# Kernel tuning notes

Measured on AMD Instinct MI355X. Metric: run time of the kernel, lower is better.

Reference implementation:

```python
import jax, jax.numpy as jnp
import numpy as np

STRIDE = 1
PADDING = 1
DILATION = 1


def setup_inputs() -> dict:
    key = jax.random.key(0)
    k1, k2 = jax.random.split(key)
    N, C_in, H, W = 32, 128, 56, 56
    C_out, ksz = 256, 3
    x = jax.random.normal(k1, (N, C_in, H, W), dtype=jnp.float32)
    # xavier_normal_ with gain sqrt(2): std = gain*sqrt(2/(fan_in+fan_out))
    fan_in = C_in * ksz * ksz
    fan_out = C_out * ksz * ksz
    std = np.sqrt(2.0) * np.sqrt(2.0 / (fan_in + fan_out))
    weight = jax.random.normal(k2, (C_out, C_in, ksz, ksz), dtype=jnp.float32) * jnp.float32(std)
    bias = jnp.zeros((C_out,), dtype=jnp.float32)
    return {"x": x, "weight": weight, "bias": bias}


def reference(x, weight, bias):
    # Faithful to conv2d(X, K, stride, padding, dilation, bias):
    # unfold (im2col) + matmul + fold is mathematically a standard cross-correlation
    # conv; expressed here with the efficient lax primitive.
    y = jax.lax.conv_general_dilated(
        x, weight,
        window_strides=(STRIDE, STRIDE),
        padding=[(PADDING, PADDING), (PADDING, PADDING)],
        rhs_dilation=(DILATION, DILATION),
        dimension_numbers=("NCHW", "OIHW", "NCHW"),
    )
    return y + bias[None, :, None, None]
```

## Files before the change

kernel.cpp:

```cpp
#include <hip/hip_runtime.h>
#include <hip/hip_bf16.h>


#define CIN   128
#define HH    56
#define WW    56
#define COUT  256
#define HW    3136
#define NIMG  32
#define NP    (NIMG * HW)
#define XPW   58
#define XPIX  (XPW * XPW)
#define XPAD_BYTES (NIMG * XPIX * CIN * 2)
#define WT_OFF     XPAD_BYTES

typedef __bf16 bf16x8 __attribute__((ext_vector_type(8)));
typedef float  f32x4  __attribute__((ext_vector_type(4)));

#define GLD16(g, l) __builtin_amdgcn_global_load_lds( \
    (const __attribute__((address_space(1))) void*)(g), \
    (__attribute__((address_space(3))) void*)(l), 16, 0, 0)

__device__ __forceinline__ unsigned pack_bf16(float a, float b) {
    return (__float_as_uint(b) & 0xFFFF0000u) | (__float_as_uint(a) >> 16);
}

__global__ __launch_bounds__(128) void prep_x(const float* __restrict__ x,
                                              __hip_bfloat16* __restrict__ xp) {
    __shared__ unsigned short t[HH * CIN];
    const int b  = blockIdx.x;
    const int n  = b / HH;
    const int y  = b - n * HH;
    const int ci = threadIdx.x;

    const float* src = x + ((size_t)(n * CIN + ci) * HW) + y * WW;
    #pragma unroll
    for (int j = 0; j < 14; ++j) {
        const float4 v = ((const float4*)src)[j];
        t[(4 * j + 0) * CIN + ci] = (unsigned short)(__float_as_uint(v.x) >> 16);
        t[(4 * j + 1) * CIN + ci] = (unsigned short)(__float_as_uint(v.y) >> 16);
        t[(4 * j + 2) * CIN + ci] = (unsigned short)(__float_as_uint(v.z) >> 16);
        t[(4 * j + 3) * CIN + ci] = (unsigned short)(__float_as_uint(v.w) >> 16);
    }

    const uint4 z = make_uint4(0, 0, 0, 0);
    if (ci < 32) {
        const int side = ci >> 4;
        const int j    = ci & 15;
        ((uint4*)(xp + ((size_t)n * XPIX + (y + 1) * XPW + side * 57) * CIN))[j] = z;
    }
    if (y == 0)
        for (int j = ci; j < 928; j += 128)
            ((uint4*)(xp + (size_t)n * XPIX * CIN))[j] = z;
    if (y == HH - 1)
        for (int j = ci; j < 928; j += 128)
            ((uint4*)(xp + ((size_t)n * XPIX + 57 * XPW) * CIN))[j] = z;

    __syncthreads();

    uint4* dst = (uint4*)(xp + ((size_t)n * XPIX + (y + 1) * XPW + 1) * CIN);
    const uint4* lsrc = (const uint4*)t;
    #pragma unroll
    for (int j = 0; j < 7; ++j)
        dst[j * 128 + ci] = lsrc[j * 128 + ci];
}

__global__ __launch_bounds__(256) void prep_w(const float* __restrict__ w,
                                              __hip_bfloat16* __restrict__ wt) {
    const int co = blockIdx.x * 2 + (threadIdx.x >> 7);
    const int ci = threadIdx.x & 127;
    const float* src = w + (size_t)(co * CIN + ci) * 9;
    #pragma unroll
    for (int tp = 0; tp < 9; ++tp)
        wt[(size_t)tp * (COUT * CIN) + co * CIN + ci] = __float2bfloat16(src[tp]);
}

__global__ __launch_bounds__(256) void conv_main(
    const char* __restrict__ xpb,
    const char* __restrict__ wtb,
    const float* __restrict__ bias,
    float* __restrict__ out)
{
    __shared__ __align__(16) char Alds[32768];
    __shared__ __align__(16) char Blds[32768];

    const int tid  = threadIdx.x;
    const int l    = tid & 63;
    const int wv   = tid >> 6;
    const int wm   = wv & 1;
    const int wn   = wv >> 1;
    const int l15  = l & 15;
    const int quad = l >> 4;

    const int idx = blockIdx.x;
    const int bm  = (idx >> 3) & 1;
    const int bn  = (idx >> 4) * 8 + (idx & 7);
    const int pbase  = bn * 128;
    const int cobase = bm * 128;

    unsigned aoff[8], boff[8];
    #pragma unroll
    for (int j = 0; j < 8; ++j) {
        const int c    = wv * 8 + j;
        const int row  = 4 * c + (l >> 4);
        const int gseg = (l & 15) ^ (row & 15);
        aoff[j] = (unsigned)((cobase + row) * 256 + gseg * 16);
        const int p   = pbase + row;
        const int n   = p / HW;
        const int rem = p - n * HW;
        const int y   = rem / WW;
        const int x   = rem - y * WW;
        boff[j] = (unsigned)((n * XPIX + y * XPW + x) * 256 + gseg * 16);
    }

    f32x4 acc[4][4];
    #pragma unroll
    for (int i = 0; i < 4; ++i)
        #pragma unroll
        for (int j = 0; j < 4; ++j)
            acc[i][j] = (f32x4){0.f, 0.f, 0.f, 0.f};

    #pragma unroll
    for (int t = 0; t < 9; ++t) {
        const int r = t / 3;
        const int s = t - 3 * r;
        const unsigned wo = (unsigned)(t * (COUT * CIN * 2));
        const unsigned bo = (unsigned)((r * XPW + s) * 256);

        __syncthreads();
        #pragma unroll
        for (int j = 0; j < 8; ++j) {
            const int c = wv * 8 + j;
            GLD16(wtb + wo + aoff[j], Alds + c * 1024);
            GLD16(xpb + bo + boff[j], Blds + c * 1024);
        }
        __syncthreads();

        #pragma unroll
        for (int kg = 0; kg < 4; ++kg) {
            bf16x8 af[4], bfr[4];
            #pragma unroll
            for (int mt = 0; mt < 4; ++mt) {
                const int row  = wm * 64 + mt * 16 + l15;
                const int segl = (kg * 4 + quad) ^ l15;
                af[mt] = *(const bf16x8*)(Alds + row * 256 + segl * 16);
            }
            #pragma unroll
            for (int nt = 0; nt < 4; ++nt) {
                const int row  = wn * 64 + nt * 16 + l15;
                const int segl = (kg * 4 + quad) ^ l15;
                bfr[nt] = *(const bf16x8*)(Blds + row * 256 + segl * 16);
            }
            #pragma unroll
            for (int mt = 0; mt < 4; ++mt)
                #pragma unroll
                for (int nt = 0; nt < 4; ++nt)
                    acc[mt][nt] = __builtin_amdgcn_mfma_f32_16x16x32_bf16(
                        af[mt], bfr[nt], acc[mt][nt], 0, 0, 0);
        }
    }

    #pragma unroll
    for (int nt = 0; nt < 4; ++nt) {
        const int pp = pbase + wn * 64 + nt * 16 + l15;
        const int n2 = pp / HW;
        const int r2 = pp - n2 * HW;
        float* ob = out + (size_t)n2 * (COUT * HW) + r2;
        #pragma unroll
        for (int mt = 0; mt < 4; ++mt) {
            const int co = cobase + wm * 64 + mt * 16 + quad * 4;
            const float4 bv = *(const float4*)(bias + co);
            f32x4 a = acc[mt][nt];
            ob[(size_t)(co + 0) * HW] = a[0] + bv.x;
            ob[(size_t)(co + 1) * HW] = a[1] + bv.y;
            ob[(size_t)(co + 2) * HW] = a[2] + bv.z;
            ob[(size_t)(co + 3) * HW] = a[3] + bv.w;
        }
    }
}

extern "C" void kernel_launch(void* const* d_in, const int* in_sizes, int n_in,
                              void* d_out, int out_size, void* d_ws, size_t ws_size,
                              hipStream_t stream) {
    const float* x = (const float*)d_in[0];
    const float* w = (const float*)d_in[1];
    const float* b = (const float*)d_in[2];
    char* ws = (char*)d_ws;
    __hip_bfloat16* xp = (__hip_bfloat16*)ws;
    __hip_bfloat16* wt = (__hip_bfloat16*)(ws + WT_OFF);

    prep_x<<<dim3(NIMG * HH), dim3(128), 0, stream>>>(x, xp);
    prep_w<<<dim3(128), dim3(256), 0, stream>>>(w, wt);
    conv_main<<<dim3((NP / 128) * 2), dim3(256), 0, stream>>>(
        (const char*)xp, (const char*)wt, b, (float*)d_out);
}
```

Measured before the change: 209.9 us.

## Pipeline conv K-loop with 4-stage LDS ring buffer and async loads

```diff
diff --git a/kernel.cpp b/kernel.cpp
--- a/kernel.cpp
+++ b/kernel.cpp
@@ -81,8 +81,7 @@
     const float* __restrict__ bias,
     float* __restrict__ out)
 {
-    __shared__ __align__(16) char Alds[32768];
-    __shared__ __align__(16) char Blds[32768];
+    __shared__ __align__(16) char L[65536];
 
     const int tid  = threadIdx.x;
     const int l    = tid & 63;
@@ -98,12 +97,12 @@
     const int pbase  = bn * 128;
     const int cobase = bm * 128;
 
-    unsigned aoff[8], boff[8];
-    #pragma unroll
-    for (int j = 0; j < 8; ++j) {
-        const int c    = wv * 8 + j;
-        const int row  = 4 * c + (l >> 4);
-        const int gseg = (l & 15) ^ (row & 15);
+    const int gseg = (l & 3) ^ ((l >> 3) & 3);
+    unsigned aoff[2], boff[2];
+    #pragma unroll
+    for (int j = 0; j < 2; ++j) {
+        const int c   = wv * 2 + j;
+        const int row = c * 16 + (l >> 2);
         aoff[j] = (unsigned)((cobase + row) * 256 + gseg * 16);
         const int p   = pbase + row;
         const int n   = p / HW;
@@ -112,6 +111,7 @@
         const int x   = rem - y * WW;
         boff[j] = (unsigned)((n * XPIX + y * XPW + x) * 256 + gseg * 16);
     }
+    const int segoff = (quad ^ ((l15 >> 1) & 3)) << 4;
 
     f32x4 acc[4][4];
     #pragma unroll
@@ -120,45 +120,56 @@
         for (int j = 0; j < 4; ++j)
             acc[i][j] = (f32x4){0.f, 0.f, 0.f, 0.f};
 
-    #pragma unroll
-    for (int t = 0; t < 9; ++t) {
-        const int r = t / 3;
-        const int s = t - 3 * r;
-        const unsigned wo = (unsigned)(t * (COUT * CIN * 2));
-        const unsigned bo = (unsigned)((r * XPW + s) * 256);
-
-        __syncthreads();
-        #pragma unroll
-        for (int j = 0; j < 8; ++j) {
-            const int c = wv * 8 + j;
-            GLD16(wtb + wo + aoff[j], Alds + c * 1024);
-            GLD16(xpb + bo + boff[j], Blds + c * 1024);
+    auto STAGE = [&](int s, int bufw) {
+        const int t  = s >> 2;
+        const int kq = s & 3;
+        const int r  = t / 3;
+        const int sx = t - 3 * r;
+        const unsigned wo = (unsigned)(t * (COUT * CIN * 2) + kq * 64);
+        const unsigned bo = (unsigned)((r * XPW + sx) * 256 + kq * 64);
+        char* Ab = L + bufw * 8192;
+        char* Bb = L + 32768 + bufw * 8192;
+        #pragma unroll
+        for (int j = 0; j < 2; ++j) {
+            const int c = wv * 2 + j;
+            GLD16(wtb + wo + aoff[j], Ab + c * 1024);
+            GLD16(xpb + bo + boff[j], Bb + c * 1024);
         }
-        __syncthreads();
-
-        #pragma unroll
-        for (int kg = 0; kg < 4; ++kg) {
-            bf16x8 af[4], bfr[4];
+    };
+
+    STAGE(0, 0);
+    STAGE(1, 1);
+    STAGE(2, 2);
+
+    #pragma unroll
+    for (int s = 0; s < 36; ++s) {
+        asm volatile("s_waitcnt vmcnt(8)" ::: "memory");
+        __builtin_amdgcn_s_barrier();
+        asm volatile("" ::: "memory");
+
+        STAGE((s + 3 < 36) ? s + 3 : 35, (s + 3) & 3);
+
+        const char* Ab = L + (s & 3) * 8192;
+        const char* Bb = L + 32768 + (s & 3) * 8192;
+        bf16x8 af[4], bfr[4];
+        #pragma unroll
+        for (int mt = 0; mt < 4; ++mt)
+            af[mt] = *(const bf16x8*)(Ab + (wm * 64 + mt * 16 + l15) * 64 + segoff);
+        #pragma unroll
+        for (int nt = 0; nt < 4; ++nt)
+            bfr[nt] = *(const bf16x8*)(Bb + (wn * 64 + nt * 16 + l15) * 64 + segoff);
+
+        __builtin_amdgcn_s_setprio(1);
+        #pragma unroll
+        for (int mt = 0; mt < 4; ++mt)
             #pragma unroll
-            for (int mt = 0; mt < 4; ++mt) {
-                const int row  = wm * 64 + mt * 16 + l15;
-                const int segl = (kg * 4 + quad) ^ l15;
-                af[mt] = *(const bf16x8*)(Alds + row * 256 + segl * 16);
-            }
-            #pragma unroll
-            for (int nt = 0; nt < 4; ++nt) {
-                const int row  = wn * 64 + nt * 16 + l15;
-                const int segl = (kg * 4 + quad) ^ l15;
-                bfr[nt] = *(const bf16x8*)(Blds + row * 256 + segl * 16);
-            }
-            #pragma unroll
-            for (int mt = 0; mt < 4; ++mt)
-                #pragma unroll
-                for (int nt = 0; nt < 4; ++nt)
-                    acc[mt][nt] = __builtin_amdgcn_mfma_f32_16x16x32_bf16(
-                        af[mt], bfr[nt], acc[mt][nt], 0, 0, 0);
-        }
-    }
+            for (int nt = 0; nt < 4; ++nt)
+                acc[mt][nt] = __builtin_amdgcn_mfma_f32_16x16x32_bf16(
+                    af[mt], bfr[nt], acc[mt][nt], 0, 0, 0);
+        __builtin_amdgcn_s_setprio(0);
+    }
+
+    asm volatile("s_waitcnt vmcnt(0)" ::: "memory");
 
     #pragma unroll
     for (int nt = 0; nt < 4; ++nt) {
```

Result: no change. 213.3 us (+1.6%).
